# Kernel tuning notes

Hardware: AMD Instinct MI355X
Metric: run time of the kernel (lower is better)

## Reference

```python
import jax, jax.numpy as jnp
import numpy as np

VAR_FLOOR = 0.002
BS, A, IN, H, L, NNH, ATT, NACT = 1024, 32, 96, 64, 16, 64, 32, 16


def _lin(x, w, b):
    return x @ w.T + b


def _lrelu(x):
    return jax.nn.leaky_relu(x, 0.01)


def setup_inputs() -> dict:
    key = jax.random.key(0)
    ks = jax.random.split(key, 24)
    def w(k, o, i):
        return jax.random.normal(k, (o, i), jnp.float32) / np.float32(np.sqrt(i))
    def b(k, o):
        return jax.random.normal(k, (o,), jnp.float32) * 0.01
    N = BS * A
    return {
        "inputs": jax.random.normal(ks[0], (N, IN), jnp.float32),
        "hidden_state": jax.random.normal(ks[1], (N, H), jnp.float32),
        "eps": jax.random.normal(ks[2], (N, A * L), jnp.float32),
        "fc1_w": w(ks[3], H, IN), "fc1_b": b(ks[4], H),
        "gru_wih": w(ks[5], 3 * H, H), "gru_whh": w(ks[6], 3 * H, H),
        "gru_bih": b(ks[7], 3 * H), "gru_bhh": b(ks[8], 3 * H),
        "fc2_w": w(ks[9], NACT, H), "fc2_b": b(ks[10], NACT),
        "emb_w1": w(ks[11], NNH, H), "emb_b1": b(ks[12], NNH),
        "bn_g": jnp.ones((NNH,), jnp.float32), "bn_b": jnp.zeros((NNH,), jnp.float32),
        "emb_w2": w(ks[13], A * L * 2, NNH), "emb_b2": b(ks[14], A * L * 2),
        "msg_w1": w(ks[15], NNH, H + L), "msg_b1": b(ks[16], NNH),
        "msg_w2": w(ks[17], NACT, NNH), "msg_b2": b(ks[18], NACT),
        "wq_w": w(ks[19], ATT, H), "wq_b": b(ks[20], ATT),
        "wk_w": w(ks[21], ATT, L), "wk_b": b(ks[22], ATT),
        "bs": BS, "t": 0,
    }


def reference(inputs, hidden_state, eps, fc1_w, fc1_b, gru_wih, gru_whh, gru_bih,
              gru_bhh, fc2_w, fc2_b, emb_w1, emb_b1, bn_g, bn_b, emb_w2, emb_b2,
              msg_w1, msg_b1, msg_w2, msg_b2, wq_w, wq_b, wk_w, wk_b, bs, t):
    Hd = fc1_w.shape[0]
    x = jax.nn.relu(_lin(inputs, fc1_w, fc1_b))
    h_in = hidden_state.reshape(-1, Hd)
    # GRUCell
    gi = _lin(x, gru_wih, gru_bih)
    gh = _lin(h_in, gru_whh, gru_bhh)
    ir, iz, inn = jnp.split(gi, 3, axis=-1)
    hr, hz, hn = jnp.split(gh, 3, axis=-1)
    r = jax.nn.sigmoid(ir + hr)
    z = jax.nn.sigmoid(iz + hz)
    n = jnp.tanh(inn + r * hn)
    h = (1.0 - z) * n + z * h_in
    q = _lin(h, fc2_w, fc2_b)
    # embed_net: Linear -> BatchNorm(train) -> LeakyReLU -> Linear
    z1 = _lin(h, emb_w1, emb_b1)
    z1 = bn_g * (z1 - z1.mean(0)) / jnp.sqrt(z1.var(0) + 1e-5) + bn_b
    lat_par = _lin(_lrelu(z1), emb_w2, emb_b2)
    D = lat_par.shape[-1] // 2
    Ld = wk_w.shape[1]
    Ag = D // Ld
    mu = lat_par[:, :D]
    var = jnp.clip(jnp.exp(lat_par[:, D:]), VAR_FLOOR, None)
    latent = (mu + jnp.sqrt(var) * eps).reshape(bs, Ag, Ag, Ld)  # [b,i,j,L]
    # msg_net on (h of receiver j, latent[b,i,j])
    h3 = h.reshape(bs, Ag, Hd)
    h_rep = jnp.broadcast_to(h3[:, None, :, :], (bs, Ag, Ag, Hd))  # [b,i,j]=h[b,j]
    msg_in = jnp.concatenate([h_rep, latent], axis=-1)
    msg = _lin(_lrelu(_lin(msg_in, msg_w1, msg_b1)), msg_w2, msg_b2)  # (b,A,A,n_act)
    # attention gating
    att = wq_w.shape[0]
    query = _lin(h, wq_w, wq_b).reshape(bs, Ag, att) / np.float32(np.sqrt(att))
    key_ = _lin(latent, wk_w, wk_b)  # (b,A,A,att)
    alpha = jnp.einsum('bia,bija->bij', query, key_)
    alpha = jnp.where(jnp.eye(Ag, dtype=bool)[None], -1e9, alpha)
    alpha = jax.nn.softmax(alpha, axis=-1)
    agg = jnp.einsum('bij,bijn->bjn', alpha, msg)  # sum gated msgs over sender i
    return_q = q + agg.reshape(bs * Ag, -1)
    return (return_q, h)
```

## Files before the change

kernel.cpp:

```cpp
#include <hip/hip_runtime.h>
#include <math.h>

namespace {

constexpr int NROW = 32768;
constexpr int HDIM = 64;
constexpr int DH   = 512;

typedef __attribute__((ext_vector_type(8))) short bf16x8;
typedef __attribute__((ext_vector_type(4))) float f32x4;
typedef __attribute__((ext_vector_type(4))) unsigned uint4e;
typedef __attribute__((ext_vector_type(2))) unsigned uint2e;

__device__ __forceinline__ float sigmoidf_(float x) { return 1.f / (1.f + __expf(-x)); }
__device__ __forceinline__ float lrelu_(float x) { return x > 0.f ? x : 0.01f * x; }
__device__ __forceinline__ unsigned pkbf(float a, float b) {
  unsigned ua = __float_as_uint(a) + 0x8000u;
  unsigned ub = __float_as_uint(b) + 0x8000u;
  return __builtin_amdgcn_perm(ub, ua, 0x07060302);
}

__global__ __launch_bounds__(512, 1) void k_fgru(
    const float* __restrict__ in,
    const float* __restrict__ hprev,
    const float* __restrict__ fc1w, const float* __restrict__ fc1b,
    const float* __restrict__ wih, const float* __restrict__ whh,
    const float* __restrict__ bih, const float* __restrict__ bhh,
    float* __restrict__ hT, float* __restrict__ hout) {
  __shared__ char smem[73728];
  const int t = threadIdx.x;
  const int n0 = blockIdx.x * 128;
  short*    xS = (short*)smem;
  unsigned* gU = (unsigned*)(smem + 18432);
  float*    trF = (float*)(smem + 18432);

  const float2* wih2 = (const float2*)wih;
  const float2* whh2 = (const float2*)whh;
  {
    float2 wv[12];
#pragma unroll
    for (int i = 0; i < 12; ++i) {
      int idx = t + 512 * i;
      int row = idx >> 5, kp = idx & 31;
      wv[i] = wih2[row * 32 + kp];
    }
#pragma unroll
    for (int i = 0; i < 12; ++i) {
      int idx = t + 512 * i;
      int row = idx >> 5, kp = idx & 31;
      int gate = row >> 6, cl = row & 63;
      gU[(gate * 64 + cl) * 36 + kp] = pkbf(wv[i].x, wv[i].y);
    }
#pragma unroll
    for (int i = 0; i < 12; ++i) {
      int idx = t + 512 * i;
      int row = idx >> 5, kp = idx & 31;
      wv[i] = whh2[row * 32 + kp];
    }
#pragma unroll
    for (int i = 0; i < 12; ++i) {
      int idx = t + 512 * i;
      int row = idx >> 5, kp = idx & 31;
      int gate = row >> 6, cl = row & 63;
      gU[((gate + 3) * 64 + cl) * 36 + kp] = pkbf(wv[i].x, wv[i].y);
    }
  }

  const int w = t >> 6, l = t & 63;
  const int m = l & 15, g = l >> 4;
  const int rowA = n0 + w * 16 + m;

  bf16x8 af[3];
#pragma unroll
  for (int ks = 0; ks < 3; ++ks) {
    const float4* p = (const float4*)(in + (size_t)rowA * 96 + ks * 32 + g * 8);
    float4 a = p[0], b = p[1];
    union { unsigned u[4]; bf16x8 h; } tw;
    tw.u[0] = pkbf(a.x, a.y); tw.u[1] = pkbf(a.z, a.w);
    tw.u[2] = pkbf(b.x, b.y); tw.u[3] = pkbf(b.z, b.w);
    af[ks] = tw.h;
  }
  {
    f32x4 accx[4];
#pragma unroll
    for (int ct = 0; ct < 4; ++ct) accx[ct] = (f32x4){0.f, 0.f, 0.f, 0.f};
#pragma unroll
    for (int ct = 0; ct < 4; ++ct)
#pragma unroll
      for (int ks = 0; ks < 3; ++ks) {
        const float4* p = (const float4*)(fc1w + (ct * 16 + m) * 96 + ks * 32 + g * 8);
        float4 a = p[0], b = p[1];
        union { unsigned u[4]; bf16x8 h; } tw;
        tw.u[0] = pkbf(a.x, a.y); tw.u[1] = pkbf(a.z, a.w);
        tw.u[2] = pkbf(b.x, b.y); tw.u[3] = pkbf(b.z, b.w);
        accx[ct] = __builtin_amdgcn_mfma_f32_16x16x32_bf16(af[ks], tw.h, accx[ct], 0, 0, 0);
      }
#pragma unroll
    for (int ct = 0; ct < 4; ++ct) {
      int c = ct * 16 + m;
      float bc = fc1b[c];
#pragma unroll
      for (int reg = 0; reg < 4; ++reg) {
        int nl = w * 16 + g * 4 + reg;
        float v = fmaxf(accx[ct][reg] + bc, 0.f);
        xS[nl * 72 + c] = (short)((__float_as_uint(v) + 0x8000u) >> 16);
      }
    }
  }
  __syncthreads();

  bf16x8 ax[2], ah[2];
#pragma unroll
  for (int ks = 0; ks < 2; ++ks) {
    ax[ks] = *(const bf16x8*)(xS + (w * 16 + m) * 72 + ks * 32 + g * 8);
    const float4* p = (const float4*)(hprev + (size_t)rowA * 64 + ks * 32 + g * 8);
    float4 a = p[0], b = p[1];
    union { unsigned u[4]; bf16x8 h; } tw;
    tw.u[0] = pkbf(a.x, a.y); tw.u[1] = pkbf(a.z, a.w);
    tw.u[2] = pkbf(b.x, b.y); tw.u[3] = pkbf(b.z, b.w);
    ah[ks] = tw.h;
  }
  const short* gS = (const short*)gU;
  float hc[4][4];
#pragma unroll 1
  for (int ct = 0; ct < 4; ++ct) {
    f32x4 a_ir = (f32x4){0.f,0.f,0.f,0.f}, a_iz = (f32x4){0.f,0.f,0.f,0.f},
          a_in = (f32x4){0.f,0.f,0.f,0.f}, a_hr = (f32x4){0.f,0.f,0.f,0.f},
          a_hz = (f32x4){0.f,0.f,0.f,0.f}, a_hn = (f32x4){0.f,0.f,0.f,0.f};
    int crow = ct * 16 + m;
#pragma unroll
    for (int ks = 0; ks < 2; ++ks) {
      bf16x8 b0 = *(const bf16x8*)(gS + (0 * 64 + crow) * 72 + ks * 32 + g * 8);
      bf16x8 b1 = *(const bf16x8*)(gS + (1 * 64 + crow) * 72 + ks * 32 + g * 8);
      bf16x8 b2 = *(const bf16x8*)(gS + (2 * 64 + crow) * 72 + ks * 32 + g * 8);
      bf16x8 b3 = *(const bf16x8*)(gS + (3 * 64 + crow) * 72 + ks * 32 + g * 8);
      bf16x8 b4 = *(const bf16x8*)(gS + (4 * 64 + crow) * 72 + ks * 32 + g * 8);
      bf16x8 b5 = *(const bf16x8*)(gS + (5 * 64 + crow) * 72 + ks * 32 + g * 8);
      a_ir = __builtin_amdgcn_mfma_f32_16x16x32_bf16(ax[ks], b0, a_ir, 0, 0, 0);
      a_iz = __builtin_amdgcn_mfma_f32_16x16x32_bf16(ax[ks], b1, a_iz, 0, 0, 0);
      a_in = __builtin_amdgcn_mfma_f32_16x16x32_bf16(ax[ks], b2, a_in, 0, 0, 0);
      a_hr = __builtin_amdgcn_mfma_f32_16x16x32_bf16(ah[ks], b3, a_hr, 0, 0, 0);
      a_hz = __builtin_amdgcn_mfma_f32_16x16x32_bf16(ah[ks], b4, a_hz, 0, 0, 0);
      a_hn = __builtin_amdgcn_mfma_f32_16x16x32_bf16(ah[ks], b5, a_hn, 0, 0, 0);
    }
    float bir = bih[crow], biz = bih[64 + crow], bin = bih[128 + crow];
    float bhr = bhh[crow], bhz = bhh[64 + crow], bhn = bhh[128 + crow];
#pragma unroll
    for (int reg = 0; reg < 4; ++reg) {
      int nl = w * 16 + g * 4 + reg;
      float hv = hprev[(size_t)(n0 + nl) * 64 + crow];
      float r  = sigmoidf_(a_ir[reg] + bir + a_hr[reg] + bhr);
      float z  = sigmoidf_(a_iz[reg] + biz + a_hz[reg] + bhz);
      float nn = tanhf(a_in[reg] + bin + r * (a_hn[reg] + bhn));
      hc[ct][reg] = (1.f - z) * nn + z * hv;
    }
  }
  __syncthreads();
#pragma unroll
  for (int ct = 0; ct < 4; ++ct)
#pragma unroll
    for (int reg = 0; reg < 4; ++reg)
      trF[(ct * 16 + m) * 133 + w * 16 + g * 4 + reg] = hc[ct][reg];
  __syncthreads();
#pragma unroll
  for (int i = 0; i < 16; ++i) {
    int idx = t + 512 * i;
    int nl = idx & 127, cl = idx >> 7;
    hT[(size_t)cl * NROW + n0 + nl] = trF[cl * 133 + nl];
  }
#pragma unroll
  for (int i = 0; i < 16; ++i) {
    int idx = t + 512 * i;
    int c = idx & 63, nl = idx >> 6;
    hout[(size_t)(n0 + nl) * 64 + c] = trF[c * 133 + nl];
  }
}

__global__ __launch_bounds__(256) void k_heads(const float* __restrict__ hT,
    const float* __restrict__ fc2w, const float* __restrict__ fc2b,
    const float* __restrict__ wqw, const float* __restrict__ wkw,
    const float* __restrict__ ew1, const float* __restrict__ eb1,
    float* __restrict__ qT, float* __restrict__ qkT, float* __restrict__ z1T,
    float* __restrict__ part) {
  __shared__ char smem[36864];
  const int t = threadIdx.x;
  const int n0 = blockIdx.x * 128;
  unsigned* hU = (unsigned*)smem;
  unsigned* wU = (unsigned*)(smem + 18432);
  float* sp1 = (float*)(smem + 18432 + 13824);
  float* sp2 = sp1 + 256;
  const float qs = 0.17677669529663687f;

  {
    float va[16], vb[16];
#pragma unroll
    for (int i = 0; i < 16; ++i) {
      int idx = t + 256 * i;
      int nl = idx & 127, kp = idx >> 7;
      va[i] = hT[(size_t)(2 * kp) * NROW + n0 + nl];
      vb[i] = hT[(size_t)(2 * kp + 1) * NROW + n0 + nl];
    }
#pragma unroll
    for (int i = 0; i < 16; ++i) {
      int idx = t + 256 * i;
      int nl = idx & 127, kp = idx >> 7;
      hU[nl * 36 + kp] = pkbf(va[i], vb[i]);
    }
  }
  {
    float2 wv[10];
#pragma unroll
    for (int i = 0; i < 10; ++i) {
      int idx = t + 256 * i;
      int kp = idx & 31, cl = idx >> 5;
      const float* src = (cl < 16) ? (fc2w + cl * 64) : (ew1 + (cl - 16) * 64);
      wv[i] = *(const float2*)(src + 2 * kp);
    }
#pragma unroll
    for (int i = 0; i < 10; ++i) {
      int idx = t + 256 * i;
      int kp = idx & 31, cl = idx >> 5;
      int dst = (cl < 16) ? cl : (cl + 16);
      wU[dst * 36 + kp] = pkbf(wv[i].x, wv[i].y);
    }
  }
  {
    int kp = t & 31, ll = t >> 5;
#pragma unroll
    for (int h = 0; h < 2; ++h) {
      int row = ll + 8 * h;
      float s0 = 0.f, s1 = 0.f;
#pragma unroll
      for (int a = 0; a < 32; ++a) {
        float wk = wkw[a * 16 + row];
        s0 = fmaf(wk, wqw[a * 64 + 2 * kp], s0);
        s1 = fmaf(wk, wqw[a * 64 + 2 * kp + 1], s1);
      }
      wU[(16 + row) * 36 + kp] = pkbf(s0 * qs, s1 * qs);
    }
  }
  __syncthreads();

  const int w = t >> 6, l = t & 63;
  const int m = l & 15, g = l >> 4;
  const short* sH = (const short*)hU;
  const short* sW = (const short*)wU;

  bf16x8 af[2][2];
#pragma unroll
  for (int mt = 0; mt < 2; ++mt)
#pragma unroll
    for (int ks = 0; ks < 2; ++ks)
      af[mt][ks] = *(const bf16x8*)(sH + (w * 32 + mt * 16 + m) * 72 + ks * 32 + g * 8);

  f32x4 acc[2][6];
#pragma unroll
  for (int mt = 0; mt < 2; ++mt)
#pragma unroll
    for (int ct = 0; ct < 6; ++ct) acc[mt][ct] = (f32x4){0.f, 0.f, 0.f, 0.f};
#pragma unroll
  for (int ct = 0; ct < 6; ++ct)
#pragma unroll
    for (int ks = 0; ks < 2; ++ks) {
      bf16x8 bw = *(const bf16x8*)(sW + (ct * 16 + m) * 72 + ks * 32 + g * 8);
#pragma unroll
      for (int mt = 0; mt < 2; ++mt)
        acc[mt][ct] = __builtin_amdgcn_mfma_f32_16x16x32_bf16(af[mt][ks], bw, acc[mt][ct], 0, 0, 0);
    }

  float s1[4], s2[4];
#pragma unroll
  for (int zt = 0; zt < 4; ++zt) { s1[zt] = 0.f; s2[zt] = 0.f; }
#pragma unroll
  for (int mt = 0; mt < 2; ++mt) {
    int nb = n0 + w * 32 + mt * 16 + g * 4;
    {
      float bc = fc2b[m];
      f32x4 v;
#pragma unroll
      for (int reg = 0; reg < 4; ++reg) v[reg] = acc[mt][0][reg] + bc;
      *(f32x4*)(qT + (size_t)m * NROW + nb) = v;
    }
    *(f32x4*)(qkT + (size_t)m * NROW + nb) = acc[mt][1];
#pragma unroll
    for (int ct = 2; ct < 6; ++ct) {
      int z = (ct - 2) * 16 + m;
      float bc = eb1[z];
      f32x4 v;
#pragma unroll
      for (int reg = 0; reg < 4; ++reg) {
        float zv = acc[mt][ct][reg] + bc;
        v[reg] = zv;
        s1[ct - 2] += zv;
        s2[ct - 2] = fmaf(zv, zv, s2[ct - 2]);
      }
      *(f32x4*)(z1T + (size_t)z * NROW + nb) = v;
    }
  }
#pragma unroll
  for (int zt = 0; zt < 4; ++zt) {
    s1[zt] += __shfl_down(s1[zt], 16, 64);
    s1[zt] += __shfl_down(s1[zt], 32, 64);
    s2[zt] += __shfl_down(s2[zt], 16, 64);
    s2[zt] += __shfl_down(s2[zt], 32, 64);
  }
  if (l < 16) {
#pragma unroll
    for (int zt = 0; zt < 4; ++zt) {
      sp1[w * 64 + zt * 16 + m] = s1[zt];
      sp2[w * 64 + zt * 16 + m] = s2[zt];
    }
  }
  __syncthreads();
  if (t < 64) {
    float a1 = sp1[t] + sp1[64 + t] + sp1[128 + t] + sp1[192 + t];
    float a2 = sp2[t] + sp2[64 + t] + sp2[128 + t] + sp2[192 + t];
    part[(size_t)blockIdx.x * 128 + t] = a1;
    part[(size_t)blockIdx.x * 128 + 64 + t] = a2;
  }
}

__global__ __launch_bounds__(256) void k_bnstat(const float* __restrict__ part,
    const float* __restrict__ bng, const float* __restrict__ bnb,
    float* __restrict__ stat) {
  __shared__ float red[512];
  const int t = threadIdx.x;
  const int c = t & 63, q = t >> 6;
  float s1 = 0.f, s2 = 0.f;
#pragma unroll 4
  for (int b = q; b < 256; b += 4) {
    s1 += part[(size_t)b * 128 + c];
    s2 += part[(size_t)b * 128 + 64 + c];
  }
  red[q * 64 + c] = s1;
  red[256 + q * 64 + c] = s2;
  __syncthreads();
  if (t < 64) {
    float a1 = red[t] + red[64 + t] + red[128 + t] + red[192 + t];
    float a2 = red[256 + t] + red[320 + t] + red[384 + t] + red[448 + t];
    float mean = a1 * (1.f / NROW);
    float var = a2 * (1.f / NROW) - mean * mean;
    float rstd = rsqrtf(var + 1e-5f);
    float sc = bng[t] * rstd;
    stat[t] = sc;
    stat[64 + t] = bnb[t] - mean * sc;
  }
}

__global__ __launch_bounds__(512, 4) void k_emb_gemm(const float* __restrict__ z1T,
    const float* __restrict__ stat,
    const float* __restrict__ ew2, const float* __restrict__ eb2,
    const float* __restrict__ eps,
    unsigned* __restrict__ latB16g) {
  __shared__ char smem[73728];
  const int t = threadIdx.x;
  const int nb = blockIdx.x >> 1;
  const int half = blockIdx.x & 1;
  const int n0 = nb * 128;
  const int ch0 = half * 256;

  unsigned* aU = (unsigned*)smem;
  unsigned* wB0 = (unsigned*)(smem + 18432);
  unsigned* wB1 = (unsigned*)(smem + 36864);
  unsigned* wB2 = (unsigned*)(smem + 55296);

  const int w = t >> 6, l = t & 63;
  const int m = l & 15, g = l >> 4;
  const float4* ew2_4 = (const float4*)ew2;
  const float stdfloor = 0.04472135955f;
  const int rowG = n0 + w * 16 + g * 4;
  const int kp4 = t & 15, cl = t >> 4;

  float4 wmA, wmB, wlA, wlB;
  float epsC[16], epsN[16], epsT[16];

  auto loadW = [&](int c2) {
    wmA = ew2_4[(size_t)(c2 + cl) * 16 + kp4];
    wmB = ew2_4[(size_t)(c2 + 32 + cl) * 16 + kp4];
    wlA = ew2_4[(size_t)(512 + c2 + cl) * 16 + kp4];
    wlB = ew2_4[(size_t)(512 + c2 + 32 + cl) * 16 + kp4];
  };
  auto packW = [&](unsigned* bp) {
    *(uint2e*)(bp + cl * 36 + kp4 * 2) = (uint2e){pkbf(wmA.x, wmA.y), pkbf(wmA.z, wmA.w)};
    *(uint2e*)(bp + (32 + cl) * 36 + kp4 * 2) = (uint2e){pkbf(wmB.x, wmB.y), pkbf(wmB.z, wmB.w)};
    *(uint2e*)(bp + (64 + cl) * 36 + kp4 * 2) = (uint2e){pkbf(wlA.x, wlA.y), pkbf(wlA.z, wlA.w)};
    *(uint2e*)(bp + (96 + cl) * 36 + kp4 * 2) = (uint2e){pkbf(wlB.x, wlB.y), pkbf(wlB.z, wlB.w)};
  };
  auto loadE = [&](int c0v, float* arr) {
#pragma unroll
    for (int ct = 0; ct < 4; ++ct)
#pragma unroll
      for (int reg = 0; reg < 4; ++reg)
        arr[ct * 4 + reg] = eps[(size_t)(rowG + reg) * 512 + c0v + ct * 16 + m];
  };

  {
    float va[8], vb[8];
#pragma unroll
    for (int i = 0; i < 8; ++i) {
      int idx = t + 512 * i;
      int nl = idx & 127, kp = idx >> 7;
      va[i] = z1T[(size_t)(2 * kp) * NROW + n0 + nl];
      vb[i] = z1T[(size_t)(2 * kp + 1) * NROW + n0 + nl];
    }
#pragma unroll
    for (int i = 0; i < 8; ++i) {
      int idx = t + 512 * i;
      int nl = idx & 127, kp = idx >> 7;
      float v0 = lrelu_(fmaf(stat[2 * kp], va[i], stat[64 + 2 * kp]));
      float v1 = lrelu_(fmaf(stat[2 * kp + 1], vb[i], stat[64 + 2 * kp + 1]));
      aU[nl * 36 + kp] = pkbf(v0, v1);
    }
  }
  loadW(ch0);
  packW(wB0);
  loadW(ch0 + 64);
  loadE(ch0, epsC);
  loadE(ch0 + 64, epsN);
  __syncthreads();

  const short* sA = (const short*)aU;
  bf16x8 af[2];
#pragma unroll
  for (int ks = 0; ks < 2; ++ks)
    af[ks] = *(const bf16x8*)(sA + (w * 16 + m) * 72 + ks * 32 + g * 8);

  auto compute = [&](const unsigned* wbu, int c0, const float* epsArr) {
    const short* sW = (const short*)wbu;
    f32x4 accm[4], accl[4];
#pragma unroll
    for (int ct = 0; ct < 4; ++ct) {
      accm[ct] = (f32x4){0.f, 0.f, 0.f, 0.f};
      accl[ct] = (f32x4){0.f, 0.f, 0.f, 0.f};
    }
#pragma unroll
    for (int ct = 0; ct < 4; ++ct)
#pragma unroll
      for (int ks = 0; ks < 2; ++ks) {
        bf16x8 bm = *(const bf16x8*)(sW + (ct * 16 + m) * 72 + ks * 32 + g * 8);
        bf16x8 bl = *(const bf16x8*)(sW + (64 + ct * 16 + m) * 72 + ks * 32 + g * 8);
        accm[ct] = __builtin_amdgcn_mfma_f32_16x16x32_bf16(af[ks], bm, accm[ct], 0, 0, 0);
        accl[ct] = __builtin_amdgcn_mfma_f32_16x16x32_bf16(af[ks], bl, accl[ct], 0, 0, 0);
      }
#pragma unroll
    for (int ct = 0; ct < 4; ++ct) {
      int c = c0 + ct * 16 + m;
      float ebm = eb2[c], ebl = eb2[DH + c];
#pragma unroll
      for (int reg = 0; reg < 4; ++reg) {
        float mu = accm[ct][reg] + ebm;
        float lv = accl[ct][reg] + ebl;
        float sd = fmaxf(__expf(0.5f * lv), stdfloor);
        float lat = fmaf(sd, epsArr[ct * 4 + reg], mu);
        float lat2 = __shfl_xor(lat, 1, 64);
        if (!(m & 1)) {
          latB16g[(size_t)(rowG + reg) * 256 + (c0 >> 1) + ct * 8 + (m >> 1)] =
              pkbf(lat, lat2);
        }
      }
    }
  };

  packW(wB1);
  __syncthreads();
  loadW(ch0 + 128);
  loadE(ch0 + 128, epsT);
  compute(wB0, ch0, epsC);
#pragma unroll
  for (int i = 0; i < 16; ++i) { epsC[i] = epsN[i]; epsN[i] = epsT[i]; }
  packW(wB2);
  __syncthreads();
  loadW(ch0 + 192);
  loadE(ch0 + 192, epsT);
  compute(wB1, ch0 + 64, epsC);
#pragma unroll
  for (int i = 0; i < 16; ++i) { epsC[i] = epsN[i]; epsN[i] = epsT[i]; }
  packW(wB0);
  __syncthreads();
  compute(wB2, ch0 + 128, epsC);
#pragma unroll
  for (int i = 0; i < 16; ++i) epsC[i] = epsN[i];
  compute(wB0, ch0 + 192, epsC);
}

constexpr int LATB_OFF = 0;
constexpr int H3B_OFF  = 40960;
constexpr int W1H_OFF  = 45568;
constexpr int W1L_OFF  = 54784;
constexpr int W2P_OFF  = 57344;
constexpr int ALL_OFF  = 59648;
constexpr int MT_OFF   = 63872;
constexpr int QKL_OFF  = 74112;
__global__ __launch_bounds__(256, 1) void k_msg(
    const unsigned* __restrict__ latB16g, const float* __restrict__ qkT,
    const float* __restrict__ qT, const float* __restrict__ hrow,
    const float* __restrict__ w1, const float* __restrict__ b1,
    const float* __restrict__ w2, const float* __restrict__ b2,
    float* __restrict__ out) {
  __shared__ char smem[76672];
  const int t = threadIdx.x;
  const int b = blockIdx.x;
  const int b32 = b * 32;
  unsigned* latB_dw = (unsigned*)(smem + LATB_OFF);

  {
    const uint4e* g4 = (const uint4e*)latB16g + (size_t)b32 * 64;
#pragma unroll
    for (int half = 0; half < 2; ++half) {
      uint4e v[4];
#pragma unroll
      for (int it = 0; it < 4; ++it) v[it] = g4[t + 256 * (4 * half + it)];
#pragma unroll
      for (int it = 0; it < 4; ++it) {
        int idx = t + 256 * (4 * half + it);
        int i = idx >> 6;
        int rem = idx & 63;
        int j = rem >> 1, hh = rem & 1;
        unsigned* dst = latB_dw + (i * 32 + j) * 10 + hh * 4;
        *(uint2e*)dst = (uint2e){v[it].x, v[it].y};
        *(uint2e*)(dst + 2) = (uint2e){v[it].z, v[it].w};
      }
    }
  }
  {
    float* qkL = (float*)(smem + QKL_OFF);
    int i = t & 31;
    float v0 = qkT[(size_t)((t >> 5)) * NROW + b32 + i];
    float v1 = qkT[(size_t)((t >> 5) + 8) * NROW + b32 + i];
    qkL[i * 20 + (t >> 5)] = v0;
    qkL[i * 20 + (t >> 5) + 8] = v1;
  }
  {
    int cp = t & 31, jj = t >> 5;
    const float2* h2 = (const float2*)hrow;
    float2 hv[4];
#pragma unroll
    for (int it = 0; it < 4; ++it)
      hv[it] = h2[((size_t)(b32 + jj + 8 * it) * 64 + 2 * cp) >> 1];
    unsigned* dst = (unsigned*)(smem + H3B_OFF);
#pragma unroll
    for (int it = 0; it < 4; ++it)
      dst[(jj + 8 * it) * 36 + cp] = pkbf(hv[it].x, hv[it].y);
  }
  {
    int kp = t & 31, cc = t >> 5;
    const float2* w12 = (const float2*)w1;
    float2 wv[8];
#pragma unroll
    for (int it = 0; it < 8; ++it)
      wv[it] = w12[((cc + 8 * it) * 80 + 2 * kp) >> 1];
    unsigned* dst = (unsigned*)(smem + W1H_OFF);
#pragma unroll
    for (int it = 0; it < 8; ++it)
      dst[(cc + 8 * it) * 36 + kp] = pkbf(wv[it].x, wv[it].y);
  }
  {
    int lp = t & 7, cc = t >> 3;
    const float2* w12 = (const float2*)w1;
    float2 wv[2];
#pragma unroll
    for (int it = 0; it < 2; ++it)
      wv[it] = w12[((cc + 32 * it) * 80 + 64 + 2 * lp) >> 1];
    unsigned* dst = (unsigned*)(smem + W1L_OFF);
#pragma unroll
    for (int it = 0; it < 2; ++it)
      dst[(cc + 32 * it) * 10 + lp] = pkbf(wv[it].x, wv[it].y);
  }
  {
    int pp = t & 31, nn = t >> 5;
    const float2* w22 = (const float2*)w2;
    int p = 2 * pp;
    int c = ((p >> 2) & 3) * 16 + (p >> 4) * 4 + (p & 3);
    float2 wv0 = w22[(nn * 64 + c) >> 1];
    float2 wv1 = w22[((nn + 8) * 64 + c) >> 1];
    unsigned* dst = (unsigned*)(smem + W2P_OFF);
    dst[nn * 36 + pp] = pkbf(wv0.x, wv0.y);
    dst[(nn + 8) * 36 + pp] = pkbf(wv1.x, wv1.y);
  }
  __syncthreads();

  {
    const float* qkL = (const float*)(smem + QKL_OFF);
    float* alL = (float*)(smem + ALL_OFF);
#pragma unroll 1
    for (int p = 0; p < 4; ++p) {
      int i = (t >> 5) + 8 * p;
      int j = t & 31;
      const unsigned* lr = latB_dw + (i * 32 + j) * 10;
      float acc = 0.f;
#pragma unroll
      for (int d = 0; d < 8; ++d) {
        unsigned u = lr[d];
        float lo = __uint_as_float(u << 16);
        float hi = __uint_as_float(u & 0xffff0000u);
        acc = fmaf(lo, qkL[i * 20 + 2 * d], acc);
        acc = fmaf(hi, qkL[i * 20 + 2 * d + 1], acc);
      }
      if (j == i) acc = -1e9f;
      float mx = acc;
#pragma unroll
      for (int msk = 16; msk > 0; msk >>= 1) mx = fmaxf(mx, __shfl_xor(mx, msk, 32));
      float e = __expf(acc - mx);
      float s = e;
#pragma unroll
      for (int msk = 16; msk > 0; msk >>= 1) s += __shfl_xor(s, msk, 32);
      alL[i * 33 + j] = e / s;
    }
  }

  const int w = t >> 6, l = t & 63;
  const int n15 = l & 15, q = l >> 4;
  const int jh = w & 1, ibase = (w >> 1) * 16;
  const bool kact = (q < 2);

  f32x4 hp[4];
#pragma unroll
  for (int ct = 0; ct < 4; ++ct) hp[ct] = (f32x4){0.f, 0.f, 0.f, 0.f};
#pragma unroll
  for (int ct = 0; ct < 4; ++ct)
#pragma unroll
    for (int ks = 0; ks < 2; ++ks) {
      bf16x8 aF = *(const bf16x8*)(smem + W1H_OFF + (ct * 16 + n15) * 144 + ks * 64 + q * 16);
      bf16x8 bF = *(const bf16x8*)(smem + H3B_OFF + (jh * 16 + n15) * 144 + ks * 64 + q * 16);
      hp[ct] = __builtin_amdgcn_mfma_f32_16x16x32_bf16(aF, bF, hp[ct], 0, 0, 0);
    }
#pragma unroll
  for (int ct = 0; ct < 4; ++ct)
#pragma unroll
    for (int reg = 0; reg < 4; ++reg)
      hp[ct][reg] += b1[ct * 16 + q * 4 + reg];

  bf16x8 aL[4];
#pragma unroll
  for (int ct = 0; ct < 4; ++ct) {
    union { unsigned u[4]; bf16x8 h; } tmp;
    tmp.u[0] = tmp.u[1] = tmp.u[2] = tmp.u[3] = 0u;
    if (kact) {
      const unsigned* p = (const unsigned*)(smem + W1L_OFF) + (ct * 16 + n15) * 10 + q * 4;
      uint2e d0 = *(const uint2e*)p;
      uint2e d1 = *(const uint2e*)(p + 2);
      tmp.u[0] = d0.x; tmp.u[1] = d0.y; tmp.u[2] = d1.x; tmp.u[3] = d1.y;
    }
    aL[ct] = tmp.h;
  }
  bf16x8 w2F[2];
#pragma unroll
  for (int ks = 0; ks < 2; ++ks)
    w2F[ks] = *(const bf16x8*)(smem + W2P_OFF + n15 * 144 + ks * 64 + q * 16);
  float b2v[4];
#pragma unroll
  for (int reg = 0; reg < 4; ++reg) b2v[reg] = b2[q * 4 + reg];

  __syncthreads();

  float agg[4] = {0.f, 0.f, 0.f, 0.f};
  char* wb = smem + MT_OFF + w * 2560;
  const float* alLf = (const float*)(smem + ALL_OFF);
#pragma unroll 1
  for (int it = 0; it < 16; ++it) {
    int ii = ibase + it;
    int r = ii * 32 + jh * 16 + n15;
    union { unsigned u[4]; bf16x8 h; } latF;
    latF.u[0] = latF.u[1] = latF.u[2] = latF.u[3] = 0u;
    if (kact) {
      const unsigned* p = latB_dw + r * 10 + q * 4;
      uint2e d0 = *(const uint2e*)p;
      uint2e d1 = *(const uint2e*)(p + 2);
      latF.u[0] = d0.x; latF.u[1] = d0.y; latF.u[2] = d1.x; latF.u[3] = d1.y;
    }
    f32x4 acc[4];
#pragma unroll
    for (int ct = 0; ct < 4; ++ct) {
      acc[ct] = (f32x4){0.f, 0.f, 0.f, 0.f};
      acc[ct] = __builtin_amdgcn_mfma_f32_16x16x32_bf16(aL[ct], latF.h, acc[ct], 0, 0, 0);
    }
#pragma unroll
    for (int h = 0; h < 2; ++h) {
      float m0[4], m1[4];
#pragma unroll
      for (int reg = 0; reg < 4; ++reg) {
        float v0 = acc[2 * h][reg] + hp[2 * h][reg];
        float v1 = acc[2 * h + 1][reg] + hp[2 * h + 1][reg];
        m0[reg] = fmaxf(v0, 0.01f * v0);
        m1[reg] = fmaxf(v1, 0.01f * v1);
      }
      uint4e pk4;
      pk4.x = pkbf(m0[0], m0[1]); pk4.y = pkbf(m0[2], m0[3]);
      pk4.z = pkbf(m1[0], m1[1]); pk4.w = pkbf(m1[2], m1[3]);
      int qp = (2 * q + h) & 3;
      *(uint4e*)(wb + (q >> 1) * 1280 + n15 * 80 + qp * 16) = pk4;
    }
    f32x4 msg = (f32x4){0.f, 0.f, 0.f, 0.f};
#pragma unroll
    for (int ks = 0; ks < 2; ++ks) {
      bf16x8 mF = *(const bf16x8*)(wb + ks * 1280 + n15 * 80 + q * 16);
      msg = __builtin_amdgcn_mfma_f32_16x16x32_bf16(w2F[ks], mF, msg, 0, 0, 0);
    }
    float aw = alLf[ii * 33 + jh * 16 + n15];
#pragma unroll
    for (int reg = 0; reg < 4; ++reg)
      agg[reg] = fmaf(aw, msg[reg] + b2v[reg], agg[reg]);
  }
  {
    f32x4 av; av[0] = agg[0]; av[1] = agg[1]; av[2] = agg[2]; av[3] = agg[3];
    *(f32x4*)(wb + n15 * 80 + q * 16) = av;
  }
  __syncthreads();
#pragma unroll
  for (int tt = 0; tt < 2; ++tt) {
    int idx = t + 256 * tt;
    int jg = idx >> 4, nn = idx & 15;
    int jh2 = jg >> 4, jl = jg & 15;
    float a0 = *(const float*)(smem + MT_OFF + jh2 * 2560 + jl * 80 + nn * 4);
    float a1 = *(const float*)(smem + MT_OFF + (jh2 + 2) * 2560 + jl * 80 + nn * 4);
    out[(size_t)b * 512 + idx] = a0 + a1 + qT[(size_t)nn * NROW + b32 + jg];
  }
}

}

extern "C" void kernel_launch(void* const* d_in, const int* in_sizes, int n_in,
                              void* d_out, int out_size, void* d_ws, size_t ws_size,
                              hipStream_t stream) {
  (void)in_sizes; (void)n_in; (void)out_size; (void)ws_size;
  const float* inputs = (const float*)d_in[0];
  const float* hidden = (const float*)d_in[1];
  const float* eps    = (const float*)d_in[2];
  const float* fc1w   = (const float*)d_in[3];
  const float* fc1b   = (const float*)d_in[4];
  const float* wih    = (const float*)d_in[5];
  const float* whh    = (const float*)d_in[6];
  const float* bih    = (const float*)d_in[7];
  const float* bhh    = (const float*)d_in[8];
  const float* fc2w   = (const float*)d_in[9];
  const float* fc2b   = (const float*)d_in[10];
  const float* ew1    = (const float*)d_in[11];
  const float* eb1    = (const float*)d_in[12];
  const float* bng    = (const float*)d_in[13];
  const float* bnb    = (const float*)d_in[14];
  const float* ew2    = (const float*)d_in[15];
  const float* eb2    = (const float*)d_in[16];
  const float* w1     = (const float*)d_in[17];
  const float* b1     = (const float*)d_in[18];
  const float* w2     = (const float*)d_in[19];
  const float* b2     = (const float*)d_in[20];
  const float* wqw    = (const float*)d_in[21];
  const float* wkw    = (const float*)d_in[23];

  float* ws = (float*)d_ws;
  float* hT     = ws;
  float* qT     = ws + 2097152;
  float* qkT    = ws + 2621440;
  float* z1T    = ws + 3670016;
  float* part   = ws + 5767168;
  float* stat   = ws + 5832704;
  unsigned* latB16g = (unsigned*)(ws + 5832832);

  float* out_q = (float*)d_out;
  float* out_h = (float*)d_out + 524288;

  hipLaunchKernelGGL(k_fgru, dim3(256), dim3(512), 0, stream,
                     inputs, hidden, fc1w, fc1b, wih, whh, bih, bhh, hT, out_h);
  hipLaunchKernelGGL(k_heads, dim3(256), dim3(256), 0, stream,
                     hT, fc2w, fc2b, wqw, wkw, ew1, eb1, qT, qkT, z1T, part);
  hipLaunchKernelGGL(k_bnstat, dim3(1), dim3(256), 0, stream, part, bng, bnb, stat);
  hipLaunchKernelGGL(k_emb_gemm, dim3(512), dim3(512), 0, stream, z1T, stat, ew2, eb2, eps, latB16g);
  hipLaunchKernelGGL(k_msg, dim3(1024), dim3(256), 0, stream,
                     latB16g, qkT, qT, out_h, w1, b1, w2, b2, out_q);
}
```

Baseline: 256.8 us.

## Fuse embedding GEMM and latent sampling into message kernel, pre-pack weights to bf16

The separate k_emb_gemm kernel is removed. Each k_msg block now computes its 32 rows of latent samples directly into shared memory, using BN-normalised z1 and bf16 weights. The k_bnstat launch gains extra blocks that convert emb_w2 to bf16 once. This drops the global latent round-trip (32768x512 bf16 written then re-read) and one launch. In exchange, k_msg runs a per-block GEMM that reads eps and the weights from global, and its shared-memory reuse of the MT region must not conflict with later stages.

```diff
diff --git a/kernel.cpp b/kernel.cpp
--- a/kernel.cpp
+++ b/kernel.cpp
@@ -322,165 +322,43 @@
 
 __global__ __launch_bounds__(256) void k_bnstat(const float* __restrict__ part,
     const float* __restrict__ bng, const float* __restrict__ bnb,
-    float* __restrict__ stat) {
-  __shared__ float red[512];
-  const int t = threadIdx.x;
-  const int c = t & 63, q = t >> 6;
-  float s1 = 0.f, s2 = 0.f;
+    const float* __restrict__ ew2,
+    float* __restrict__ stat, unsigned* __restrict__ ew2b) {
+  if (blockIdx.x == 0) {
+    __shared__ float red[512];
+    const int t = threadIdx.x;
+    const int c = t & 63, q = t >> 6;
+    float s1 = 0.f, s2 = 0.f;
 #pragma unroll 4
-  for (int b = q; b < 256; b += 4) {
-    s1 += part[(size_t)b * 128 + c];
-    s2 += part[(size_t)b * 128 + 64 + c];
-  }
-  red[q * 64 + c] = s1;
-  red[256 + q * 64 + c] = s2;
-  __syncthreads();
-  if (t < 64) {
-    float a1 = red[t] + red[64 + t] + red[128 + t] + red[192 + t];
-    float a2 = red[256 + t] + red[320 + t] + red[384 + t] + red[448 + t];
-    float mean = a1 * (1.f / NROW);
-    float var = a2 * (1.f / NROW) - mean * mean;
-    float rstd = rsqrtf(var + 1e-5f);
-    float sc = bng[t] * rstd;
-    stat[t] = sc;
-    stat[64 + t] = bnb[t] - mean * sc;
-  }
-}
-
-__global__ __launch_bounds__(512, 4) void k_emb_gemm(const float* __restrict__ z1T,
-    const float* __restrict__ stat,
-    const float* __restrict__ ew2, const float* __restrict__ eb2,
-    const float* __restrict__ eps,
-    unsigned* __restrict__ latB16g) {
-  __shared__ char smem[73728];
-  const int t = threadIdx.x;
-  const int nb = blockIdx.x >> 1;
-  const int half = blockIdx.x & 1;
-  const int n0 = nb * 128;
-  const int ch0 = half * 256;
-
-  unsigned* aU = (unsigned*)smem;
-  unsigned* wB0 = (unsigned*)(smem + 18432);
-  unsigned* wB1 = (unsigned*)(smem + 36864);
-  unsigned* wB2 = (unsigned*)(smem + 55296);
-
-  const int w = t >> 6, l = t & 63;
-  const int m = l & 15, g = l >> 4;
-  const float4* ew2_4 = (const float4*)ew2;
-  const float stdfloor = 0.04472135955f;
-  const int rowG = n0 + w * 16 + g * 4;
-  const int kp4 = t & 15, cl = t >> 4;
-
-  float4 wmA, wmB, wlA, wlB;
-  float epsC[16], epsN[16], epsT[16];
-
-  auto loadW = [&](int c2) {
-    wmA = ew2_4[(size_t)(c2 + cl) * 16 + kp4];
-    wmB = ew2_4[(size_t)(c2 + 32 + cl) * 16 + kp4];
-    wlA = ew2_4[(size_t)(512 + c2 + cl) * 16 + kp4];
-    wlB = ew2_4[(size_t)(512 + c2 + 32 + cl) * 16 + kp4];
-  };
-  auto packW = [&](unsigned* bp) {
-    *(uint2e*)(bp + cl * 36 + kp4 * 2) = (uint2e){pkbf(wmA.x, wmA.y), pkbf(wmA.z, wmA.w)};
-    *(uint2e*)(bp + (32 + cl) * 36 + kp4 * 2) = (uint2e){pkbf(wmB.x, wmB.y), pkbf(wmB.z, wmB.w)};
-    *(uint2e*)(bp + (64 + cl) * 36 + kp4 * 2) = (uint2e){pkbf(wlA.x, wlA.y), pkbf(wlA.z, wlA.w)};
-    *(uint2e*)(bp + (96 + cl) * 36 + kp4 * 2) = (uint2e){pkbf(wlB.x, wlB.y), pkbf(wlB.z, wlB.w)};
-  };
-  auto loadE = [&](int c0v, float* arr) {
-#pragma unroll
-    for (int ct = 0; ct < 4; ++ct)
-#pragma unroll
-      for (int reg = 0; reg < 4; ++reg)
-        arr[ct * 4 + reg] = eps[(size_t)(rowG + reg) * 512 + c0v + ct * 16 + m];
-  };
-
-  {
-    float va[8], vb[8];
-#pragma unroll
-    for (int i = 0; i < 8; ++i) {
-      int idx = t + 512 * i;
-      int nl = idx & 127, kp = idx >> 7;
-      va[i] = z1T[(size_t)(2 * kp) * NROW + n0 + nl];
-      vb[i] = z1T[(size_t)(2 * kp + 1) * NROW + n0 + nl];
-    }
-#pragma unroll
-    for (int i = 0; i < 8; ++i) {
-      int idx = t + 512 * i;
-      int nl = idx & 127, kp = idx >> 7;
-      float v0 = lrelu_(fmaf(stat[2 * kp], va[i], stat[64 + 2 * kp]));
-      float v1 = lrelu_(fmaf(stat[2 * kp + 1], vb[i], stat[64 + 2 * kp + 1]));
-      aU[nl * 36 + kp] = pkbf(v0, v1);
-    }
-  }
-  loadW(ch0);
-  packW(wB0);
-  loadW(ch0 + 64);
-  loadE(ch0, epsC);
-  loadE(ch0 + 64, epsN);
-  __syncthreads();
-
-  const short* sA = (const short*)aU;
-  bf16x8 af[2];
-#pragma unroll
-  for (int ks = 0; ks < 2; ++ks)
-    af[ks] = *(const bf16x8*)(sA + (w * 16 + m) * 72 + ks * 32 + g * 8);
-
-  auto compute = [&](const unsigned* wbu, int c0, const float* epsArr) {
-    const short* sW = (const short*)wbu;
-    f32x4 accm[4], accl[4];
-#pragma unroll
-    for (int ct = 0; ct < 4; ++ct) {
-      accm[ct] = (f32x4){0.f, 0.f, 0.f, 0.f};
-      accl[ct] = (f32x4){0.f, 0.f, 0.f, 0.f};
-    }
-#pragma unroll
-    for (int ct = 0; ct < 4; ++ct)
-#pragma unroll
-      for (int ks = 0; ks < 2; ++ks) {
-        bf16x8 bm = *(const bf16x8*)(sW + (ct * 16 + m) * 72 + ks * 32 + g * 8);
-        bf16x8 bl = *(const bf16x8*)(sW + (64 + ct * 16 + m) * 72 + ks * 32 + g * 8);
-        accm[ct] = __builtin_amdgcn_mfma_f32_16x16x32_bf16(af[ks], bm, accm[ct], 0, 0, 0);
-        accl[ct] = __builtin_amdgcn_mfma_f32_16x16x32_bf16(af[ks], bl, accl[ct], 0, 0, 0);
-      }
-#pragma unroll
-    for (int ct = 0; ct < 4; ++ct) {
-      int c = c0 + ct * 16 + m;
-      float ebm = eb2[c], ebl = eb2[DH + c];
-#pragma unroll
-      for (int reg = 0; reg < 4; ++reg) {
-        float mu = accm[ct][reg] + ebm;
-        float lv = accl[ct][reg] + ebl;
-        float sd = fmaxf(__expf(0.5f * lv), stdfloor);
-        float lat = fmaf(sd, epsArr[ct * 4 + reg], mu);
-        float lat2 = __shfl_xor(lat, 1, 64);
-        if (!(m & 1)) {
-          latB16g[(size_t)(rowG + reg) * 256 + (c0 >> 1) + ct * 8 + (m >> 1)] =
-              pkbf(lat, lat2);
-        }
-      }
-    }
-  };
-
-  packW(wB1);
-  __syncthreads();
-  loadW(ch0 + 128);
-  loadE(ch0 + 128, epsT);
-  compute(wB0, ch0, epsC);
-#pragma unroll
-  for (int i = 0; i < 16; ++i) { epsC[i] = epsN[i]; epsN[i] = epsT[i]; }
-  packW(wB2);
-  __syncthreads();
-  loadW(ch0 + 192);
-  loadE(ch0 + 192, epsT);
-  compute(wB1, ch0 + 64, epsC);
-#pragma unroll
-  for (int i = 0; i < 16; ++i) { epsC[i] = epsN[i]; epsN[i] = epsT[i]; }
-  packW(wB0);
-  __syncthreads();
-  compute(wB2, ch0 + 128, epsC);
-#pragma unroll
-  for (int i = 0; i < 16; ++i) epsC[i] = epsN[i];
-  compute(wB0, ch0 + 192, epsC);
+    for (int b = q; b < 256; b += 4) {
+      s1 += part[(size_t)b * 128 + c];
+      s2 += part[(size_t)b * 128 + 64 + c];
+    }
+    red[q * 64 + c] = s1;
+    red[256 + q * 64 + c] = s2;
+    __syncthreads();
+    if (t < 64) {
+      float a1 = red[t] + red[64 + t] + red[128 + t] + red[192 + t];
+      float a2 = red[256 + t] + red[320 + t] + red[384 + t] + red[448 + t];
+      float mean = a1 * (1.f / NROW);
+      float var = a2 * (1.f / NROW) - mean * mean;
+      float rstd = rsqrtf(var + 1e-5f);
+      float sc = bng[t] * rstd;
+      stat[t] = sc;
+      stat[64 + t] = bnb[t] - mean * sc;
+    }
+  } else {
+    const int rb = blockIdx.x - 1;
+    const int t = threadIdx.x;
+#pragma unroll
+    for (int it = 0; it < 2; ++it) {
+      int id2 = t + 256 * it;
+      int r = rb * 16 + (id2 >> 5);
+      int cp = id2 & 31;
+      float2 v = *(const float2*)(ew2 + (size_t)r * 64 + 2 * cp);
+      ew2b[(size_t)r * 32 + cp] = pkbf(v.x, v.y);
+    }
+  }
 }
 
 constexpr int LATB_OFF = 0;
@@ -492,7 +370,10 @@
 constexpr int MT_OFF   = 63872;
 constexpr int QKL_OFF  = 74112;
 __global__ __launch_bounds__(256, 1) void k_msg(
-    const unsigned* __restrict__ latB16g, const float* __restrict__ qkT,
+    const unsigned* __restrict__ ew2b, const float* __restrict__ stat,
+    const float* __restrict__ z1T, const float* __restrict__ eb2,
+    const float* __restrict__ eps,
+    const float* __restrict__ qkT,
     const float* __restrict__ qT, const float* __restrict__ hrow,
     const float* __restrict__ w1, const float* __restrict__ b1,
     const float* __restrict__ w2, const float* __restrict__ b2,
@@ -503,23 +384,24 @@
   const int b32 = b * 32;
   unsigned* latB_dw = (unsigned*)(smem + LATB_OFF);
 
-  {
-    const uint4e* g4 = (const uint4e*)latB16g + (size_t)b32 * 64;
-#pragma unroll
-    for (int half = 0; half < 2; ++half) {
-      uint4e v[4];
-#pragma unroll
-      for (int it = 0; it < 4; ++it) v[it] = g4[t + 256 * (4 * half + it)];
-#pragma unroll
-      for (int it = 0; it < 4; ++it) {
-        int idx = t + 256 * (4 * half + it);
-        int i = idx >> 6;
-        int rem = idx & 63;
-        int j = rem >> 1, hh = rem & 1;
-        unsigned* dst = latB_dw + (i * 32 + j) * 10 + hh * 4;
-        *(uint2e*)dst = (uint2e){v[it].x, v[it].y};
-        *(uint2e*)(dst + 2) = (uint2e){v[it].z, v[it].w};
-      }
+  const int w = t >> 6, l = t & 63;
+  const int m = l & 15, g = l >> 4;
+
+  {
+    short* xz = (short*)(smem + MT_OFF);
+    float zv[8];
+#pragma unroll
+    for (int it = 0; it < 8; ++it) {
+      int idx = t + 256 * it;
+      int i = idx & 31, c = idx >> 5;
+      zv[it] = z1T[(size_t)c * NROW + b32 + i];
+    }
+#pragma unroll
+    for (int it = 0; it < 8; ++it) {
+      int idx = t + 256 * it;
+      int i = idx & 31, c = idx >> 5;
+      float v = lrelu_(fmaf(stat[c], zv[it], stat[64 + c]));
+      xz[i * 72 + c] = (short)((__float_as_uint(v) + 0x8000u) >> 16);
     }
   }
   {
@@ -580,6 +462,64 @@
   __syncthreads();
 
   {
+    const short* xzS = (const short*)(smem + MT_OFF);
+    bf16x8 afz[2][2];
+#pragma unroll
+    for (int mt = 0; mt < 2; ++mt)
+#pragma unroll
+      for (int ks = 0; ks < 2; ++ks)
+        afz[mt][ks] = *(const bf16x8*)(xzS + (mt * 16 + m) * 72 + ks * 32 + g * 8);
+    const uint4e* w4 = (const uint4e*)ew2b;
+    const float stdfloor = 0.04472135955f;
+#pragma unroll 2
+    for (int ci8 = 0; ci8 < 8; ++ci8) {
+      int ci = w * 8 + ci8;
+      int c = ci * 16 + m;
+      union { uint4e u; bf16x8 h; } bmu[2], blv[2];
+#pragma unroll
+      for (int ks = 0; ks < 2; ++ks) {
+        bmu[ks].u = w4[(size_t)(ci * 16 + m) * 8 + ks * 4 + g];
+        blv[ks].u = w4[(size_t)(512 + ci * 16 + m) * 8 + ks * 4 + g];
+      }
+      float ep[2][4];
+#pragma unroll
+      for (int mt = 0; mt < 2; ++mt)
+#pragma unroll
+        for (int reg = 0; reg < 4; ++reg)
+          ep[mt][reg] = eps[(size_t)(b32 + mt * 16 + g * 4 + reg) * 512 + c];
+      f32x4 accm[2], accl[2];
+#pragma unroll
+      for (int mt = 0; mt < 2; ++mt) {
+        accm[mt] = (f32x4){0.f, 0.f, 0.f, 0.f};
+        accl[mt] = (f32x4){0.f, 0.f, 0.f, 0.f};
+      }
+#pragma unroll
+      for (int ks = 0; ks < 2; ++ks)
+#pragma unroll
+        for (int mt = 0; mt < 2; ++mt) {
+          accm[mt] = __builtin_amdgcn_mfma_f32_16x16x32_bf16(afz[mt][ks], bmu[ks].h, accm[mt], 0, 0, 0);
+          accl[mt] = __builtin_amdgcn_mfma_f32_16x16x32_bf16(afz[mt][ks], blv[ks].h, accl[mt], 0, 0, 0);
+        }
+      float ebm = eb2[c], ebl = eb2[DH + c];
+#pragma unroll
+      for (int mt = 0; mt < 2; ++mt)
+#pragma unroll
+        for (int reg = 0; reg < 4; ++reg) {
+          float mu = accm[mt][reg] + ebm;
+          float lv = accl[mt][reg] + ebl;
+          float sd = fmaxf(__expf(0.5f * lv), stdfloor);
+          float lat = fmaf(sd, ep[mt][reg], mu);
+          float lat2 = __shfl_xor(lat, 1, 64);
+          if (!(m & 1)) {
+            int i = mt * 16 + g * 4 + reg;
+            latB_dw[(i * 32 + ci) * 10 + (m >> 1)] = pkbf(lat, lat2);
+          }
+        }
+    }
+  }
+  __syncthreads();
+
+  {
     const float* qkL = (const float*)(smem + QKL_OFF);
     float* alL = (float*)(smem + ALL_OFF);
 #pragma unroll 1
@@ -608,7 +548,6 @@
     }
   }
 
-  const int w = t >> 6, l = t & 63;
   const int n15 = l & 15, q = l >> 4;
   const int jh = w & 1, ibase = (w >> 1) * 16;
   const bool kact = (q < 2);
@@ -754,7 +693,7 @@
   float* z1T    = ws + 3670016;
   float* part   = ws + 5767168;
   float* stat   = ws + 5832704;
-  unsigned* latB16g = (unsigned*)(ws + 5832832);
+  unsigned* ew2b = (unsigned*)(ws + 5832832);
 
   float* out_q = (float*)d_out;
   float* out_h = (float*)d_out + 524288;
@@ -763,8 +702,7 @@
                      inputs, hidden, fc1w, fc1b, wih, whh, bih, bhh, hT, out_h);
   hipLaunchKernelGGL(k_heads, dim3(256), dim3(256), 0, stream,
                      hT, fc2w, fc2b, wqw, wkw, ew1, eb1, qT, qkT, z1T, part);
-  hipLaunchKernelGGL(k_bnstat, dim3(1), dim3(256), 0, stream, part, bng, bnb, stat);
-  hipLaunchKernelGGL(k_emb_gemm, dim3(512), dim3(512), 0, stream, z1T, stat, ew2, eb2, eps, latB16g);
+  hipLaunchKernelGGL(k_bnstat, dim3(65), dim3(256), 0, stream, part, bng, bnb, ew2, stat, ew2b);
   hipLaunchKernelGGL(k_msg, dim3(1024), dim3(256), 0, stream,
-                     latB16g, qkT, qT, out_h, w1, b1, w2, b2, out_q);
+                     ew2b, stat, z1T, eb2, eps, qkT, qT, out_h, w1, b1, w2, b2, out_q);
 }
```

After: 238.7 us. -7.0%, faster.
